# Kernel tuning notes

Measured on AMD Instinct MI355X. Metric: run time of the kernel, lower is better.

The kernel has to match this reference:

```python
import jax, jax.numpy as jnp
import numpy as np

N_NODES = 8192
D = 384
N_EDGES = 262144
N_REL = 4
N_LAYERS = 2
BATCH = 64


def setup_inputs() -> dict:
    key = jax.random.key(0)
    ks = jax.random.split(key, 8)
    x = jax.random.normal(ks[0], (N_NODES, D), jnp.float32)
    edge_index = jax.random.randint(ks[1], (2, N_EDGES), 0, N_NODES, dtype=jnp.int32)
    edge_type = jax.random.randint(ks[2], (N_EDGES,), 0, N_REL, dtype=jnp.int32)
    s = 1.0 / np.sqrt(D)
    W_rel = jax.random.uniform(ks[3], (N_LAYERS, N_REL, D, D), jnp.float32, -s, s)
    b_rel = jnp.zeros((N_LAYERS, N_REL, D), jnp.float32)
    norm_const = jnp.ones((N_LAYERS, N_REL), jnp.float32)
    W_msg = jax.random.uniform(ks[4], (N_LAYERS, D, D), jnp.float32, -s, s)
    b_msg = jnp.zeros((N_LAYERS, D), jnp.float32)
    W_self = jax.random.uniform(ks[5], (N_LAYERS, D, D), jnp.float32, -s, s)
    b_self = jnp.zeros((N_LAYERS, D), jnp.float32)
    bn_gamma = jnp.ones((D,), jnp.float32)
    bn_beta = jnp.zeros((D,), jnp.float32)
    return {"x": x, "edge_index": edge_index, "edge_type": edge_type,
            "bn_gamma": bn_gamma, "bn_beta": bn_beta,
            "W_rel": W_rel, "b_rel": b_rel, "norm_const": norm_const,
            "W_msg": W_msg, "b_msg": b_msg, "W_self": W_self, "b_self": b_self,
            "batch_size": BATCH}


def _seg_sum(v, idx, n):
    return jax.ops.segment_sum(v, idx, num_segments=n)


def _forward(x, bn_gamma, bn_beta, W_rel, b_rel, norm_const, W_msg, b_msg,
             W_self, b_self, edge_index, edge_type, batch_size):
    n = x.shape[0]
    # BatchNorm1d (training-mode batch stats) on the utterance embeddings
    mu = x.mean(axis=0)
    var = x.var(axis=0)
    h = bn_gamma * (x - mu) * jax.lax.rsqrt(var + 1e-5) + bn_beta
    src, dst = edge_index[0], edge_index[1]  # PyG: row=source(j), col=target(i)
    # pairwise cosine similarity, gathered only at the edges actually used:
    # edge_weights[dst, src] = <h_dst, h_src> / (|h_dst||h_src|)
    xn = h / jnp.linalg.norm(h, axis=1, keepdims=True)
    w_e = jnp.sum(xn[dst] * xn[src], axis=-1)  # [E]
    ones_e = jnp.ones(src.shape[0], jnp.float32)
    n_layers, n_rel = W_rel.shape[0], W_rel.shape[1]
    for l in range(n_layers):
        # RelationAwareMP: per-relation linear + weighted scatter-mean, summed
        out = jnp.zeros((n, W_rel.shape[2]), h.dtype)
        for r in range(n_rel):
            mask = (edge_type == r).astype(h.dtype)  # [E]
            xr = h @ W_rel[l, r].T + b_rel[l, r]  # [N, D]
            coef = mask * w_e / norm_const[l, r]  # [E]
            s = _seg_sum(coef[:, None] * xr[src], dst, n)
            c = _seg_sum(mask, dst, n)
            out = out + s / jnp.maximum(c, 1.0)[:, None]
        rel_out = jax.nn.relu(out)
        # MP: relu(mean_j lin(x_j) + self_lin(x)), then residual
        mj = rel_out @ W_msg[l].T + b_msg[l]
        s = _seg_sum(mj[src], dst, n)
        c = _seg_sum(ones_e, dst, n)
        aggr = s / jnp.maximum(c, 1.0)[:, None]
        h = jax.nn.relu(aggr + rel_out @ W_self[l].T + b_self[l]) + h
    return h.reshape(batch_size, -1, h.shape[-1]).mean(axis=1)


def reference(x, edge_index, edge_type, bn_gamma, bn_beta, W_rel, b_rel,
              norm_const, W_msg, b_msg, W_self, b_self, batch_size):
    return _forward(x, bn_gamma, bn_beta, W_rel, b_rel, norm_const,
                    W_msg, b_msg, W_self, b_self,
                    edge_index, edge_type, batch_size)
```

## Files before the change

### kernel.cpp

```cpp
#include <hip/hip_runtime.h>
#include <hip/hip_bf16.h>

#define NN 8192
#define DD 384
#define NE 262144
#define NR 4
#define NL 2
#define NB 64

typedef __attribute__((ext_vector_type(8))) short bf16x8;
typedef __attribute__((ext_vector_type(4))) float f32x4;

__device__ __forceinline__ unsigned short f2bf(float f) {
  unsigned u = __float_as_uint(f);
  unsigned r = (u + 0x7fffu + ((u >> 16) & 1u)) >> 16;
  return (unsigned short)r;
}
__device__ __forceinline__ unsigned pack_bf2(float lo, float hi) {
  return (unsigned)f2bf(lo) | ((unsigned)f2bf(hi) << 16);
}
__device__ __forceinline__ float bflo(unsigned u) { return __uint_as_float(u << 16); }
__device__ __forceinline__ float bfhi(unsigned u) { return __uint_as_float(u & 0xffff0000u); }
__device__ __forceinline__ void gl_lds16(const void* g, void* l) {
  __builtin_amdgcn_global_load_lds(
      (const __attribute__((address_space(1))) unsigned int*)g,
      (__attribute__((address_space(3))) unsigned int*)l, 16, 0, 0);
}
__device__ __forceinline__ float dot8(uint4 a, uint4 b) {
  return bflo(a.x) * bflo(b.x) + bfhi(a.x) * bfhi(b.x) +
         bflo(a.y) * bflo(b.y) + bfhi(a.y) * bfhi(b.y) +
         bflo(a.z) * bflo(b.z) + bfhi(a.z) * bfhi(b.z) +
         bflo(a.w) * bflo(b.w) + bfhi(a.w) * bfhi(b.w);
}

__global__ void k_zero(uint4* __restrict__ p, int n4) {
  int i = blockIdx.x * 256 + threadIdx.x;
  if (i < n4) p[i] = make_uint4(0, 0, 0, 0);
}

__global__ void k_colstats(const float* __restrict__ x, float* __restrict__ musum,
                           float* __restrict__ msqsum) {
  int c = threadIdx.x;
  int r0 = blockIdx.x * 32;
  float s = 0.f, s2 = 0.f;
  for (int r = 0; r < 32; ++r) {
    float v = x[(size_t)(r0 + r) * DD + c];
    s += v; s2 += v * v;
  }
  atomicAdd(&musum[c], s);
  atomicAdd(&msqsum[c], s2);
}

__global__ void k_bn(const float* __restrict__ x, const float* __restrict__ gamma,
                     const float* __restrict__ beta, const float* __restrict__ musum,
                     const float* __restrict__ msqsum, float* __restrict__ h,
                     short* __restrict__ h_bf, float* __restrict__ ninv) {
  int n = blockIdx.x;
  int t = threadIdx.x;
  float ss = 0.f;
#pragma unroll
  for (int i = 0; i < 6; ++i) {
    int c = t + i * 64;
    float m = musum[c] * (1.f / NN);
    float var = msqsum[c] * (1.f / NN) - m * m;
    float v = gamma[c] * (x[(size_t)n * DD + c] - m) * rsqrtf(var + 1e-5f) + beta[c];
    h[(size_t)n * DD + c] = v;
    h_bf[(size_t)n * DD + c] = (short)f2bf(v);
    ss += v * v;
  }
#pragma unroll
  for (int m = 32; m; m >>= 1) ss += __shfl_xor(ss, m, 64);
  if (t == 0) ninv[n] = rsqrtf(ss);
}

__global__ void k_counts(const int* __restrict__ ei, const int* __restrict__ et,
                         int* __restrict__ c_rel) {
  int e = blockIdx.x * blockDim.x + threadIdx.x;
  if (e >= NE) return;
  int dst = ei[NE + e];
  atomicAdd(&c_rel[dst * NR + et[e]], 1);
}

__global__ void k_scan(const int* __restrict__ c_rel, int* __restrict__ rp2,
                       int* __restrict__ cursor) {
  __shared__ int part[1024];
  int t = threadIdx.x;
  int base = t * 32;
  int v[32]; int s = 0;
#pragma unroll
  for (int i = 0; i < 32; ++i) { v[i] = c_rel[base + i]; s += v[i]; }
  part[t] = s;
  __syncthreads();
  for (int off = 1; off < 1024; off <<= 1) {
    int add = (t >= off) ? part[t - off] : 0;
    __syncthreads();
    part[t] += add;
    __syncthreads();
  }
  int run = (t == 0) ? 0 : part[t - 1];
  if (t == 0) rp2[0] = 0;
#pragma unroll
  for (int i = 0; i < 32; ++i) {
    cursor[base + i] = run;
    run += v[i];
    rp2[base + i + 1] = run;
  }
}

__global__ void k_wefill(const short* __restrict__ hb, const float* __restrict__ ninv,
                         const int* __restrict__ ei, const int* __restrict__ et,
                         int* __restrict__ cursor, int* __restrict__ meta,
                         float* __restrict__ wsort) {
  int sl = threadIdx.x & 15;
  int grp = (blockIdx.x * blockDim.x + threadIdx.x) >> 4;
  int ngrp = (gridDim.x * blockDim.x) >> 4;
  for (int e = grp; e < NE; e += ngrp) {
    int s = ei[e], d = ei[NE + e];
    const uint4* hs = (const uint4*)(hb + (size_t)s * DD);
    const uint4* hd = (const uint4*)(hb + (size_t)d * DD);
    uint4 a0 = hs[sl], a1 = hs[16 + sl], a2 = hs[32 + sl];
    uint4 b0 = hd[sl], b1 = hd[16 + sl], b2 = hd[32 + sl];
    float acc = dot8(a0, b0) + dot8(a1, b1) + dot8(a2, b2);
#pragma unroll
    for (int m = 8; m; m >>= 1) acc += __shfl_xor(acc, m, 64);
    if (sl == 0) {
      int pos = atomicAdd(&cursor[d * NR + et[e]], 1);
      meta[pos] = s;
      wsort[pos] = acc * ninv[s] * ninv[d];
    }
  }
}

__global__ void k_aggrel(const short* __restrict__ hb, const int* __restrict__ rp2,
                         const int* __restrict__ meta, const float* __restrict__ wsort,
                         const float* __restrict__ nc, short* __restrict__ Agg,
                         float* __restrict__ SC, int layer) {
  int n = blockIdx.x;
  int t = threadIdx.x;
  int r = t / 96;
  int i = t - r * 96;
  int beg = rp2[n * 4 + r], end = rp2[n * 4 + r + 1];
  float a0 = 0, a1 = 0, a2 = 0, a3 = 0, s = 0;
  int e = beg;
  for (; e + 3 < end; e += 4) {
    int s0 = meta[e], s1 = meta[e + 1], s2 = meta[e + 2], s3 = meta[e + 3];
    float w0 = wsort[e], w1 = wsort[e + 1], w2 = wsort[e + 2], w3 = wsort[e + 3];
    uint2 u0 = ((const uint2*)(hb + (size_t)s0 * DD))[i];
    uint2 u1 = ((const uint2*)(hb + (size_t)s1 * DD))[i];
    uint2 u2 = ((const uint2*)(hb + (size_t)s2 * DD))[i];
    uint2 u3 = ((const uint2*)(hb + (size_t)s3 * DD))[i];
    a0 += w0 * bflo(u0.x) + w1 * bflo(u1.x) + w2 * bflo(u2.x) + w3 * bflo(u3.x);
    a1 += w0 * bfhi(u0.x) + w1 * bfhi(u1.x) + w2 * bfhi(u2.x) + w3 * bfhi(u3.x);
    a2 += w0 * bflo(u0.y) + w1 * bflo(u1.y) + w2 * bflo(u2.y) + w3 * bflo(u3.y);
    a3 += w0 * bfhi(u0.y) + w1 * bfhi(u1.y) + w2 * bfhi(u2.y) + w3 * bfhi(u3.y);
    s += w0 + w1 + w2 + w3;
  }
  for (; e < end; ++e) {
    int s0 = meta[e];
    float w0 = wsort[e];
    uint2 u0 = ((const uint2*)(hb + (size_t)s0 * DD))[i];
    a0 += w0 * bflo(u0.x); a1 += w0 * bfhi(u0.x);
    a2 += w0 * bflo(u0.y); a3 += w0 * bfhi(u0.y);
    s += w0;
  }
  int c = end - beg;
  float f = 1.f / (nc[layer * 4 + r] * (float)(c > 1 ? c : 1));
  uint2 o;
  o.x = pack_bf2(a0 * f, a1 * f);
  o.y = pack_bf2(a2 * f, a3 * f);
  ((uint2*)(Agg + (size_t)n * 1536 + r * 384))[i] = o;
  if (i == 0) SC[n * 4 + r] = s * f;
}

__global__ void k_aggmp(short* __restrict__ B1, const int* __restrict__ rp2,
                        const int* __restrict__ meta) {
  __shared__ float red[3][96][4];
  int n = blockIdx.x;
  int t = threadIdx.x;
  int g = t / 96, i = t - g * 96;
  int beg = rp2[n * 4], end = rp2[n * 4 + 4];
  float a0 = 0, a1 = 0, a2 = 0, a3 = 0;
  int e = beg + g;
  for (; e + 12 < end; e += 16) {
    int s0 = meta[e], s1 = meta[e + 4], s2 = meta[e + 8], s3 = meta[e + 12];
    uint2 u0 = ((const uint2*)(B1 + (size_t)s0 * 768 + 384))[i];
    uint2 u1 = ((const uint2*)(B1 + (size_t)s1 * 768 + 384))[i];
    uint2 u2 = ((const uint2*)(B1 + (size_t)s2 * 768 + 384))[i];
    uint2 u3 = ((const uint2*)(B1 + (size_t)s3 * 768 + 384))[i];
    a0 += bflo(u0.x) + bflo(u1.x) + bflo(u2.x) + bflo(u3.x);
    a1 += bfhi(u0.x) + bfhi(u1.x) + bfhi(u2.x) + bfhi(u3.x);
    a2 += bflo(u0.y) + bflo(u1.y) + bflo(u2.y) + bflo(u3.y);
    a3 += bfhi(u0.y) + bfhi(u1.y) + bfhi(u2.y) + bfhi(u3.y);
  }
  for (; e < end; e += 4) {
    int s0 = meta[e];
    uint2 u = ((const uint2*)(B1 + (size_t)s0 * 768 + 384))[i];
    a0 += bflo(u.x); a1 += bfhi(u.x);
    a2 += bflo(u.y); a3 += bfhi(u.y);
  }
  if (g) {
    red[g - 1][i][0] = a0; red[g - 1][i][1] = a1;
    red[g - 1][i][2] = a2; red[g - 1][i][3] = a3;
  }
  __syncthreads();
  if (g == 0) {
#pragma unroll
    for (int k = 0; k < 3; ++k) {
      a0 += red[k][i][0]; a1 += red[k][i][1];
      a2 += red[k][i][2]; a3 += red[k][i][3];
    }
    float inv = (end > beg) ? 1.f / (float)(end - beg) : 0.f;
    uint2 o;
    o.x = pack_bf2(a0 * inv, a1 * inv);
    o.y = pack_bf2(a2 * inv, a3 * inv);
    ((uint2*)(B1 + (size_t)n * 768))[i] = o;
  }
}

__global__ void k_packall(const float* __restrict__ W_rel, const float* __restrict__ W_msg,
                          const float* __restrict__ W_self, short* __restrict__ Wcat,
                          short* __restrict__ Wcat2) {
  const int T1 = NL * 384 * 1536;
  const int T2 = NL * 384 * 768;
  int idx = blockIdx.x * blockDim.x + threadIdx.x;
  if (idx < T1) {
    int l = idx / (384 * 1536);
    int rem = idx - l * 384 * 1536;
    int i = rem / 1536, kk = rem - i * 1536;
    int r = kk / 384, k = kk - r * 384;
    Wcat[idx] = (short)f2bf(W_rel[(((size_t)(l * NR + r) * DD) + i) * DD + k]);
  } else if (idx < T1 + T2) {
    int j = idx - T1;
    int l = j / (384 * 768);
    int rem = j - l * 384 * 768;
    int i = rem / 768, kk = rem - i * 768;
    float v = (kk < 384) ? W_msg[((size_t)l * DD + i) * DD + kk]
                         : W_self[((size_t)l * DD + i) * DD + kk - 384];
    Wcat2[j] = (short)f2bf(v);
  }
}

template <int MODE>
__global__ __launch_bounds__(256) void k_gemm_mfma(
    const short* __restrict__ A, int K, const short* __restrict__ Bp,
    const float* __restrict__ SC, const float* __restrict__ brel_l,
    const float* __restrict__ bmsg_l, const float* __restrict__ bself_l,
    const int* __restrict__ rp2, float* __restrict__ h,
    short* __restrict__ h_bf, short* __restrict__ Cout) {
  __shared__ short As[64 * 64];
  __shared__ short Bs[64 * 64];
  int tid = threadIdx.x;
  int lane = tid & 63;
  int w = tid >> 6;
  int wr = w >> 1, wc = w & 1;
  int bm = blockIdx.x, bn = blockIdx.y;

  int r0 = (w << 3) + (lane >> 3);
  int qg = (lane & 7) ^ (r0 & 7);
  const short* Ag0 = A + (size_t)(bm * 64 + r0) * K + qg * 8;
  const short* Ag1 = A + (size_t)(bm * 64 + r0 + 32) * K + qg * 8;
  const short* Bg0 = Bp + (size_t)(bn * 64 + r0) * K + qg * 8;
  const short* Bg1 = Bp + (size_t)(bn * 64 + r0 + 32) * K + qg * 8;
  short* Asl0 = As + w * 512;
  short* Asl1 = As + 2048 + w * 512;
  short* Bsl0 = Bs + w * 512;
  short* Bsl1 = Bs + 2048 + w * 512;

  f32x4 acc[2][2] = {};
  int fr = lane & 15, fq = lane >> 4;
  for (int k0 = 0; k0 < K; k0 += 64) {
    __syncthreads();
    gl_lds16(Ag0 + k0, Asl0);
    gl_lds16(Ag1 + k0, Asl1);
    gl_lds16(Bg0 + k0, Bsl0);
    gl_lds16(Bg1 + k0, Bsl1);
    __syncthreads();
#pragma unroll
    for (int kk = 0; kk < 2; ++kk) {
      bf16x8 a[2], b[2];
#pragma unroll
      for (int i = 0; i < 2; ++i) {
        int r = wr * 32 + i * 16 + fr;
        int qs = (kk * 4 + fq) ^ (r & 7);
        a[i] = *(const bf16x8*)&As[r * 64 + qs * 8];
      }
#pragma unroll
      for (int j = 0; j < 2; ++j) {
        int r = wc * 32 + j * 16 + fr;
        int qs = (kk * 4 + fq) ^ (r & 7);
        b[j] = *(const bf16x8*)&Bs[r * 64 + qs * 8];
      }
#pragma unroll
      for (int i = 0; i < 2; ++i)
#pragma unroll
        for (int j = 0; j < 2; ++j)
          acc[i][j] = __builtin_amdgcn_mfma_f32_16x16x32_bf16(a[i], b[j], acc[i][j], 0, 0, 0);
    }
  }

  int cr = (lane >> 4) * 4;
  int cc = lane & 15;
#pragma unroll
  for (int i = 0; i < 2; ++i) {
#pragma unroll
    for (int jj = 0; jj < 4; ++jj) {
      int row = bm * 64 + wr * 32 + i * 16 + cr + jj;
      if (MODE == 0) {
        float4 sc = *(const float4*)&SC[row * 4];
#pragma unroll
        for (int j = 0; j < 2; ++j) {
          int col = bn * 64 + wc * 32 + j * 16 + cc;
          float v = acc[i][j][jj] + sc.x * brel_l[col] + sc.y * brel_l[384 + col] +
                    sc.z * brel_l[768 + col] + sc.w * brel_l[1152 + col];
          Cout[(size_t)row * 768 + 384 + col] = (short)f2bf(fmaxf(v, 0.f));
        }
      } else {
        float bmul = (rp2[(row + 1) * 4] > rp2[row * 4]) ? 1.f : 0.f;
#pragma unroll
        for (int j = 0; j < 2; ++j) {
          int col = bn * 64 + wc * 32 + j * 16 + cc;
          float v = acc[i][j][jj] + bmul * bmsg_l[col] + bself_l[col];
          float o = fmaxf(v, 0.f) + h[(size_t)row * DD + col];
          h[(size_t)row * DD + col] = o;
          h_bf[(size_t)row * DD + col] = (short)f2bf(o);
        }
      }
    }
  }
}

__global__ void k_out(const float* __restrict__ h, float* __restrict__ out) {
  int b = blockIdx.x;
  int c = threadIdx.x;
  float s = 0.f;
  for (int j = 0; j < 128; ++j) s += h[(size_t)(b * 128 + j) * DD + c];
  out[b * DD + c] = s * (1.f / 128.f);
}

extern "C" void kernel_launch(void* const* d_in, const int* in_sizes, int n_in,
                              void* d_out, int out_size, void* d_ws, size_t ws_size,
                              hipStream_t stream) {
  const float* x      = (const float*)d_in[0];
  const int*   ei     = (const int*)d_in[1];
  const int*   et     = (const int*)d_in[2];
  const float* gamma  = (const float*)d_in[3];
  const float* beta   = (const float*)d_in[4];
  const float* W_rel  = (const float*)d_in[5];
  const float* b_rel  = (const float*)d_in[6];
  const float* nc     = (const float*)d_in[7];
  const float* W_msg  = (const float*)d_in[8];
  const float* b_msg  = (const float*)d_in[9];
  const float* W_self = (const float*)d_in[10];
  const float* b_self = (const float*)d_in[11];
  float* out = (float*)d_out;

  char* ws = (char*)d_ws;
  size_t off = 0;
  auto alloc = [&](size_t bytes) -> void* {
    void* p = ws + off;
    off = (off + bytes + 255) & ~(size_t)255;
    return p;
  };
  float* h      = (float*)alloc((size_t)NN * DD * 4);
  short* h_bf   = (short*)alloc((size_t)NN * DD * 2);
  short* Agg    = (short*)alloc((size_t)NN * 1536 * 2);
  short* B1     = (short*)alloc((size_t)NN * 768 * 2);
  short* Wcat   = (short*)alloc((size_t)NL * 384 * 1536 * 2);
  short* Wcat2  = (short*)alloc((size_t)NL * 384 * 768 * 2);
  float* SC     = (float*)alloc((size_t)NN * 4 * 4);
  int*   meta   = (int*)alloc((size_t)NE * 4);
  float* wsort  = (float*)alloc((size_t)NE * 4);
  int*   rp2    = (int*)alloc((size_t)(NN * 4 + 1) * 4);
  int*   cursor = (int*)alloc((size_t)NN * 4 * 4);
  float* ninv   = (float*)alloc((size_t)NN * 4);
  char*  zb     = (char*)alloc(134144);
  float* musum  = (float*)(zb);
  float* msqsum = (float*)(zb + 1536);
  int*   c_rel  = (int*)(zb + 3072);

  k_zero<<<(134144 / 16 + 255) / 256, 256, 0, stream>>>((uint4*)zb, 134144 / 16);
  k_colstats<<<256, 384, 0, stream>>>(x, musum, msqsum);
  k_bn<<<NN, 64, 0, stream>>>(x, gamma, beta, musum, msqsum, h, h_bf, ninv);
  k_counts<<<NE / 256, 256, 0, stream>>>(ei, et, c_rel);
  k_scan<<<1, 1024, 0, stream>>>(c_rel, rp2, cursor);
  k_wefill<<<2048, 256, 0, stream>>>(h_bf, ninv, ei, et, cursor, meta, wsort);
  k_packall<<<(NL * 384 * 1536 + NL * 384 * 768 + 255) / 256, 256, 0, stream>>>(
      W_rel, W_msg, W_self, Wcat, Wcat2);

  for (int l = 0; l < NL; ++l) {
    k_aggrel<<<NN, 384, 0, stream>>>(h_bf, rp2, meta, wsort, nc, Agg, SC, l);
    k_gemm_mfma<0><<<dim3(128, 6), 256, 0, stream>>>(
        Agg, 1536, Wcat + (size_t)l * 384 * 1536, SC, b_rel + l * NR * DD,
        nullptr, nullptr, nullptr, nullptr, nullptr, B1);
    k_aggmp<<<NN, 384, 0, stream>>>(B1, rp2, meta);
    k_gemm_mfma<1><<<dim3(128, 6), 256, 0, stream>>>(
        B1, 768, Wcat2 + (size_t)l * 384 * 768, nullptr, nullptr,
        b_msg + l * DD, b_self + l * DD, rp2, h, h_bf, nullptr);
  }
  k_out<<<64, 384, 0, stream>>>(h, out);
}
```

Baseline: 308.3 us.

## Split edge-weight fill into CSR scatter plus per-node dot pass; double-buffer GEMM LDS

The fused edge kernel is split in two. A lightweight kernel scatters source indices into CSR order. A second kernel then computes cosine weights per destination node, loading the destination row once and reusing it for all incoming edges. Separately, the MFMA GEMM now double-buffers its LDS tiles so the next K tile's global-to-LDS load is issued before computing on the current one, which removes one barrier per iteration. This costs an extra kernel launch and double the LDS footprint, and relies on the async LDS load completing at the barrier.

```diff
diff --git a/kernel.cpp b/kernel.cpp
--- a/kernel.cpp
+++ b/kernel.cpp
@@ -107,27 +107,32 @@
   }
 }
 
-__global__ void k_wefill(const short* __restrict__ hb, const float* __restrict__ ninv,
-                         const int* __restrict__ ei, const int* __restrict__ et,
-                         int* __restrict__ cursor, int* __restrict__ meta,
-                         float* __restrict__ wsort) {
-  int sl = threadIdx.x & 15;
-  int grp = (blockIdx.x * blockDim.x + threadIdx.x) >> 4;
-  int ngrp = (gridDim.x * blockDim.x) >> 4;
-  for (int e = grp; e < NE; e += ngrp) {
-    int s = ei[e], d = ei[NE + e];
-    const uint4* hs = (const uint4*)(hb + (size_t)s * DD);
-    const uint4* hd = (const uint4*)(hb + (size_t)d * DD);
-    uint4 a0 = hs[sl], a1 = hs[16 + sl], a2 = hs[32 + sl];
-    uint4 b0 = hd[sl], b1 = hd[16 + sl], b2 = hd[32 + sl];
-    float acc = dot8(a0, b0) + dot8(a1, b1) + dot8(a2, b2);
+__global__ void k_fill(const int* __restrict__ ei, const int* __restrict__ et,
+                       int* __restrict__ cursor, int* __restrict__ meta) {
+  int e = blockIdx.x * blockDim.x + threadIdx.x;
+  if (e >= NE) return;
+  int src = ei[e], dst = ei[NE + e];
+  int pos = atomicAdd(&cursor[dst * NR + et[e]], 1);
+  meta[pos] = src;
+}
+
+__global__ void k_we2(const short* __restrict__ hb, const float* __restrict__ ninv,
+                      const int* __restrict__ rp2, const int* __restrict__ meta,
+                      float* __restrict__ wsort) {
+  int n = blockIdx.x;
+  int g = threadIdx.x >> 4, sl = threadIdx.x & 15;
+  int beg = rp2[n * 4], end = rp2[n * 4 + 4];
+  if (beg == end) return;
+  const uint4* hd = (const uint4*)(hb + (size_t)n * DD);
+  uint4 b0 = hd[sl], b1 = hd[16 + sl], b2 = hd[32 + sl];
+  float nd = ninv[n];
+  for (int s = beg + g; s < end; s += 16) {
+    int src = meta[s];
+    const uint4* hs = (const uint4*)(hb + (size_t)src * DD);
+    float acc = dot8(hs[sl], b0) + dot8(hs[16 + sl], b1) + dot8(hs[32 + sl], b2);
 #pragma unroll
     for (int m = 8; m; m >>= 1) acc += __shfl_xor(acc, m, 64);
-    if (sl == 0) {
-      int pos = atomicAdd(&cursor[d * NR + et[e]], 1);
-      meta[pos] = s;
-      wsort[pos] = acc * ninv[s] * ninv[d];
-    }
+    if (sl == 0) wsort[s] = acc * ninv[src] * nd;
   }
 }
 
@@ -247,8 +252,8 @@
     const float* __restrict__ bmsg_l, const float* __restrict__ bself_l,
     const int* __restrict__ rp2, float* __restrict__ h,
     short* __restrict__ h_bf, short* __restrict__ Cout) {
-  __shared__ short As[64 * 64];
-  __shared__ short Bs[64 * 64];
+  __shared__ short As[2][64 * 64];
+  __shared__ short Bs[2][64 * 64];
   int tid = threadIdx.x;
   int lane = tid & 63;
   int w = tid >> 6;
@@ -261,20 +266,23 @@
   const short* Ag1 = A + (size_t)(bm * 64 + r0 + 32) * K + qg * 8;
   const short* Bg0 = Bp + (size_t)(bn * 64 + r0) * K + qg * 8;
   const short* Bg1 = Bp + (size_t)(bn * 64 + r0 + 32) * K + qg * 8;
-  short* Asl0 = As + w * 512;
-  short* Asl1 = As + 2048 + w * 512;
-  short* Bsl0 = Bs + w * 512;
-  short* Bsl1 = Bs + 2048 + w * 512;
+
+  auto stage = [&](int bi, int k0) {
+    gl_lds16(Ag0 + k0, &As[bi][w * 512]);
+    gl_lds16(Ag1 + k0, &As[bi][2048 + w * 512]);
+    gl_lds16(Bg0 + k0, &Bs[bi][w * 512]);
+    gl_lds16(Bg1 + k0, &Bs[bi][2048 + w * 512]);
+  };
 
   f32x4 acc[2][2] = {};
   int fr = lane & 15, fq = lane >> 4;
-  for (int k0 = 0; k0 < K; k0 += 64) {
-    __syncthreads();
-    gl_lds16(Ag0 + k0, Asl0);
-    gl_lds16(Ag1 + k0, Asl1);
-    gl_lds16(Bg0 + k0, Bsl0);
-    gl_lds16(Bg1 + k0, Bsl1);
-    __syncthreads();
+  int nt = K >> 6;
+  stage(0, 0);
+  __syncthreads();
+  for (int t = 0; t < nt; ++t) {
+    if (t + 1 < nt) stage((t + 1) & 1, (t + 1) << 6);
+    const short* Ab = As[t & 1];
+    const short* Bb = Bs[t & 1];
 #pragma unroll
     for (int kk = 0; kk < 2; ++kk) {
       bf16x8 a[2], b[2];
@@ -282,13 +290,13 @@
       for (int i = 0; i < 2; ++i) {
         int r = wr * 32 + i * 16 + fr;
         int qs = (kk * 4 + fq) ^ (r & 7);
-        a[i] = *(const bf16x8*)&As[r * 64 + qs * 8];
+        a[i] = *(const bf16x8*)&Ab[r * 64 + qs * 8];
       }
 #pragma unroll
       for (int j = 0; j < 2; ++j) {
         int r = wc * 32 + j * 16 + fr;
         int qs = (kk * 4 + fq) ^ (r & 7);
-        b[j] = *(const bf16x8*)&Bs[r * 64 + qs * 8];
+        b[j] = *(const bf16x8*)&Bb[r * 64 + qs * 8];
       }
 #pragma unroll
       for (int i = 0; i < 2; ++i)
@@ -296,6 +304,7 @@
         for (int j = 0; j < 2; ++j)
           acc[i][j] = __builtin_amdgcn_mfma_f32_16x16x32_bf16(a[i], b[j], acc[i][j], 0, 0, 0);
     }
+    __syncthreads();
   }
 
   int cr = (lane >> 4) * 4;
@@ -383,7 +392,8 @@
   k_bn<<<NN, 64, 0, stream>>>(x, gamma, beta, musum, msqsum, h, h_bf, ninv);
   k_counts<<<NE / 256, 256, 0, stream>>>(ei, et, c_rel);
   k_scan<<<1, 1024, 0, stream>>>(c_rel, rp2, cursor);
-  k_wefill<<<2048, 256, 0, stream>>>(h_bf, ninv, ei, et, cursor, meta, wsort);
+  k_fill<<<NE / 256, 256, 0, stream>>>(ei, et, cursor, meta);
+  k_we2<<<NN, 256, 0, stream>>>(h_bf, ninv, rp2, meta, wsort);
   k_packall<<<(NL * 384 * 1536 + NL * 384 * 768 + 255) / 256, 256, 0, stream>>>(
       W_rel, W_msg, W_self, Wcat, Wcat2);
 
```

Result: no change. 304.3 us (-1.3%).
